# Performance work log

Measured on AMD Instinct MI355X. Metric: run time of the kernel, lower is better.

The kernel has to match this reference:

```python
import jax, jax.numpy as jnp
import numpy as np

B, T, D_MODEL, D_HIDDEN, MAX_SEQLEN = 4, 2048, 1024, 1024, 2048


def setup_inputs() -> dict:
    key = jax.random.key(0)
    ks = jax.random.split(key, 8)
    scale = 0.02  # keep exp() and linear outputs in a sane range
    return {
        "q": jax.random.normal(ks[0], (B, T, D_MODEL), dtype=jnp.float32),
        "k": jax.random.normal(ks[1], (B, T, D_MODEL), dtype=jnp.float32),
        "v": jax.random.normal(ks[2], (B, T, D_MODEL), dtype=jnp.float32),
        "Wq": jax.random.normal(ks[3], (D_HIDDEN, D_MODEL), dtype=jnp.float32) * scale,
        "Wk": jax.random.normal(ks[4], (D_HIDDEN, D_MODEL), dtype=jnp.float32) * scale,
        "Wv": jax.random.normal(ks[5], (D_HIDDEN, D_MODEL), dtype=jnp.float32) * scale,
        "Wo": jax.random.normal(ks[6], (D_MODEL, D_HIDDEN), dtype=jnp.float32) * scale,
        "W_bias": jax.random.normal(ks[7], (MAX_SEQLEN, MAX_SEQLEN), dtype=jnp.float32) * scale,
    }


def reference(q, k, v, Wq, Wk, Wv, Wo, W_bias):
    Ti = q.shape[1]
    Tj = k.shape[1]
    # Linear projections (torch Linear: x @ W.T), bias=False
    Q = jnp.einsum('btm,hm->bth', q, Wq)
    K = jnp.einsum('btm,hm->bth', k, Wk)
    V = jnp.einsum('btm,hm->bth', v, Wv)
    pos_bias = W_bias[:Ti, :Tj][None]              # (1, Ti, Tj)
    # Faithful to original: max over dim 0 (batch dim for K, singleton dim for pos_bias)
    max_key = jnp.max(K, axis=0, keepdims=True)    # (1, Tj, Dh)
    max_pos_bias = jnp.max(pos_bias, axis=0, keepdims=True)  # == pos_bias (dim 0 is size 1)
    exp_key = jnp.exp(K - max_key)                 # (B, Tj, Dh)
    exp_pos_bias = jnp.exp(pos_bias - max_pos_bias)  # all-ones, kept for faithfulness
    num = jnp.einsum('bij,bjd->bid', exp_pos_bias, exp_key * V)
    den = jnp.einsum('bij,bjd->bid', exp_pos_bias, exp_key)
    Yt = jax.nn.sigmoid(Q) * num / den             # (B, Ti, Dh)
    return jnp.einsum('bth,mh->btm', Yt, Wo)
```

## Files before the change

kernel.cpp:

```cpp
#include <hip/hip_runtime.h>
#include <hip/hip_bf16.h>

typedef __bf16 bf16;
typedef __bf16 bf16x8 __attribute__((ext_vector_type(8)));
typedef __bf16 bf16x4 __attribute__((ext_vector_type(4)));
typedef float f32x4 __attribute__((ext_vector_type(4)));
typedef float f32x16 __attribute__((ext_vector_type(16)));

#define B_   4
#define T_   2048
#define DM_  1024
#define DH_  1024
#define MROWS 8192

struct CvtJob { const float* src; bf16* dst; int nf4; };
struct CvtArgs { CvtJob job[7]; };

__global__ __launch_bounds__(256) void cvt_kernel(CvtArgs args) {
  CvtJob jb = args.job[blockIdx.y];
  int base = blockIdx.x * 2048;
  if (base >= jb.nf4) return;
  int t2 = threadIdx.x * 2;
  const float4* s = (const float4*)jb.src;
  float4 a[4][2];
#pragma unroll
  for (int u = 0; u < 4; ++u) {
    a[u][0] = s[base + u * 512 + t2];
    a[u][1] = s[base + u * 512 + t2 + 1];
  }
#pragma unroll
  for (int u = 0; u < 4; ++u) {
    bf16x8 o;
    o[0] = (bf16)a[u][0].x; o[1] = (bf16)a[u][0].y;
    o[2] = (bf16)a[u][0].z; o[3] = (bf16)a[u][0].w;
    o[4] = (bf16)a[u][1].x; o[5] = (bf16)a[u][1].y;
    o[6] = (bf16)a[u][1].z; o[7] = (bf16)a[u][1].w;
    *(bf16x8*)(jb.dst + ((size_t)base + u * 512 + t2) * 4) = o;
  }
}

struct GemmJob { const bf16* A; const bf16* Bw; float* Cf; bf16* Cb; int mode; };
struct GemmArgs { GemmJob job[4]; int N; int K; };

template <int MT>
__global__ __launch_bounds__(256) void gemm_bt(GemmArgs ga) {
  const GemmJob jb = ga.job[blockIdx.z];
  const int N = ga.N, K = ga.K;
  constexpr int TM = MT * 64;
  __shared__ __align__(16) bf16 As[TM * 64];
  __shared__ __align__(16) bf16 Bs[128 * 64];

  const int tid  = threadIdx.x;
  const int lane = tid & 63;
  const int wave = tid >> 6;
  const int wm   = (wave >> 1) * (MT * 32);
  const int wn   = (wave & 1) * 64;

  const int f   = blockIdx.y * 8 + blockIdx.x;
  const int xcd = f & 7;
  const int j   = f >> 3;
  const int bn  = j & 7;
  const int bm  = (j >> 3) * 8 + xcd;
  const int tileM = bm * TM;
  const int tileN = bn * 128;

  f32x16 acc[MT][2] = {};

  const int sr = lane >> 3;

  const char* pa = (const char*)(jb.A  + (size_t)tileM * K);
  const char* pb = (const char*)(jb.Bw + (size_t)tileN * K);
  unsigned int offA[MT * 2], offB[4];
#pragma unroll
  for (int l = 0; l < MT * 2; ++l) {
    int grp = wave * (MT * 2) + l;
    int sc  = (lane & 7) ^ sr ^ (grp & 7);
    offA[l] = (unsigned int)(((grp * 8 + sr) * K + sc * 8) * 2);
  }
#pragma unroll
  for (int l = 0; l < 4; ++l) {
    int grp = wave * 4 + l;
    int sc  = (lane & 7) ^ sr ^ (grp & 7);
    offB[l] = (unsigned int)(((grp * 8 + sr) * K + sc * 8) * 2);
  }

  const int half = lane >> 5;
  const int rc   = lane & 31;

  for (int k0 = 0; k0 < K; k0 += 64) {
#pragma unroll
    for (int l = 0; l < MT * 2; ++l)
      __builtin_amdgcn_global_load_lds(
          (const __attribute__((address_space(1))) void*)(pa + offA[l]),
          (__attribute__((address_space(3))) void*)&As[(wave * (MT * 2) + l) * 512],
          16, 0, 0);
#pragma unroll
    for (int l = 0; l < 4; ++l)
      __builtin_amdgcn_global_load_lds(
          (const __attribute__((address_space(1))) void*)(pb + offB[l]),
          (__attribute__((address_space(3))) void*)&Bs[(wave * 4 + l) * 512],
          16, 0, 0);
    pa += 128;
    pb += 128;
    __syncthreads();

#pragma unroll
    for (int s = 0; s < 2; ++s) {
      bf16x8 af[MT][2], bfr[2][2];
#pragma unroll
      for (int mt = 0; mt < MT; ++mt)
#pragma unroll
        for (int kk = 0; kk < 2; ++kk) {
          int row = wm + mt * 32 + rc;
          int chunk = ((s * 2 + kk) * 2 + half) ^ (row & 7) ^ ((row >> 3) & 7);
          af[mt][kk] = *(const bf16x8*)&As[row * 64 + chunk * 8];
        }
#pragma unroll
      for (int nt = 0; nt < 2; ++nt)
#pragma unroll
        for (int kk = 0; kk < 2; ++kk) {
          int row = wn + nt * 32 + rc;
          int chunk = ((s * 2 + kk) * 2 + half) ^ (row & 7) ^ ((row >> 3) & 7);
          bfr[nt][kk] = *(const bf16x8*)&Bs[row * 64 + chunk * 8];
        }
#pragma unroll
      for (int kk = 0; kk < 2; ++kk)
#pragma unroll
        for (int mt = 0; mt < MT; ++mt)
#pragma unroll
          for (int nt = 0; nt < 2; ++nt)
            acc[mt][nt] = __builtin_amdgcn_mfma_f32_32x32x16_bf16(
                af[mt][kk], bfr[nt][kk], acc[mt][nt], 0, 0, 0);
    }
    __syncthreads();
  }

  const int cn    = rc;
  const int rbase = half * 4;
  if (jb.mode == 0) {
#pragma unroll
    for (int mt = 0; mt < MT; ++mt)
#pragma unroll
      for (int nt = 0; nt < 2; ++nt)
#pragma unroll
        for (int r = 0; r < 16; ++r) {
          int row = tileM + wm + mt * 32 + rbase + (r & 3) + 8 * (r >> 2);
          int col = tileN + wn + nt * 32 + cn;
          jb.Cf[(size_t)row * N + col] = acc[mt][nt][r];
        }
  } else if (jb.mode == 1) {
#pragma unroll
    for (int mt = 0; mt < MT; ++mt)
#pragma unroll
      for (int nt = 0; nt < 2; ++nt)
#pragma unroll
        for (int r = 0; r < 16; ++r) {
          int row = tileM + wm + mt * 32 + rbase + (r & 3) + 8 * (r >> 2);
          int col = tileN + wn + nt * 32 + cn;
          jb.Cb[(size_t)row * N + col] =
              (bf16)(1.f / (1.f + __expf(-acc[mt][nt][r])));
        }
  } else {
#pragma unroll
    for (int mt = 0; mt < MT; ++mt)
#pragma unroll
      for (int nt = 0; nt < 2; ++nt)
#pragma unroll
        for (int r = 0; r < 16; ++r) {
          int row = tileM + wm + mt * 32 + rbase + (r & 3) + 8 * (r >> 2);
          int col = tileN + wn + nt * 32 + cn;
          jb.Cb[(size_t)row * N + col] = (bf16)acc[mt][nt][r];
        }
  }
}

__global__ __launch_bounds__(256) void reduce_kv(
    const bf16* __restrict__ Kb, const bf16* __restrict__ Vb,
    float* __restrict__ part) {
  __shared__ float lds[64 * 128];
  const int t = threadIdx.x;
  const int half = t >> 7;
  const int dt = t & 127;
  const int d = dt * 8;
  const int j0 = blockIdx.x * 8 + half * 4;
  const size_t bs = (size_t)T_ * DH_;
  float n[4][8] = {}, e[4][8] = {};
  for (int jj = j0; jj < j0 + 4; ++jj) {
    size_t off = (size_t)jj * DH_ + d;
    bf16x8 kk[4], vv[4];
#pragma unroll
    for (int b = 0; b < 4; ++b) {
      kk[b] = *(const bf16x8*)(Kb + off + b * bs);
      vv[b] = *(const bf16x8*)(Vb + off + b * bs);
    }
#pragma unroll
    for (int c = 0; c < 8; ++c) {
      float k0 = (float)kk[0][c], k1 = (float)kk[1][c];
      float k2 = (float)kk[2][c], k3 = (float)kk[3][c];
      float m = fmaxf(fmaxf(k0, k1), fmaxf(k2, k3));
      float w0 = __expf(k0 - m), w1 = __expf(k1 - m);
      float w2 = __expf(k2 - m), w3 = __expf(k3 - m);
      e[0][c] += w0; e[1][c] += w1; e[2][c] += w2; e[3][c] += w3;
      n[0][c] += w0 * (float)vv[0][c];
      n[1][c] += w1 * (float)vv[1][c];
      n[2][c] += w2 * (float)vv[2][c];
      n[3][c] += w3 * (float)vv[3][c];
    }
  }
  if (half) {
#pragma unroll
    for (int b = 0; b < 4; ++b)
#pragma unroll
      for (int c = 0; c < 8; ++c) {
        lds[(b * 8 + c) * 128 + dt] = n[b][c];
        lds[(32 + b * 8 + c) * 128 + dt] = e[b][c];
      }
  }
  __syncthreads();
  if (!half) {
    float* po = part + (size_t)blockIdx.x * 8192;
#pragma unroll
    for (int b = 0; b < 4; ++b)
#pragma unroll
      for (int c = 0; c < 8; ++c) {
        po[b * 1024 + d + c] = n[b][c] + lds[(b * 8 + c) * 128 + dt];
        po[4096 + b * 1024 + d + c] = e[b][c] + lds[(32 + b * 8 + c) * 128 + dt];
      }
  }
}

__global__ __launch_bounds__(256) void finish_kv(
    const float* __restrict__ part, float* __restrict__ numden) {
  __shared__ float lds[128];
  const int t = threadIdx.x;
  const int half = t >> 7;
  const int sl = t & 127;
  const int slot = blockIdx.x * 128 + sl;
  float s = 0.f;
  for (int i = half * 128; i < half * 128 + 128; i += 8) {
#pragma unroll
    for (int u = 0; u < 8; ++u)
      s += part[(size_t)(i + u) * 8192 + slot];
  }
  if (half) lds[sl] = s;
  __syncthreads();
  if (!half) numden[slot] = s + lds[sl];
}

__global__ __launch_bounds__(256) void scale_wo(
    const bf16* __restrict__ Wo, const float* __restrict__ numden,
    bf16* __restrict__ out4) {
  const int b = blockIdx.y;
  size_t i = ((size_t)blockIdx.x * 256 + threadIdx.x) * 8;
  int h = (int)(i & (DH_ - 1));
  bf16x8 w = *(const bf16x8*)(Wo + i);
  const float* nu = numden + b * DH_ + h;
  const float* de = numden + 4096 + b * DH_ + h;
  float4 n0 = *(const float4*)nu;
  float4 n1 = *(const float4*)(nu + 4);
  float4 d0 = *(const float4*)de;
  float4 d1 = *(const float4*)(de + 4);
  bf16x8 o;
  o[0] = (bf16)((float)w[0] * n0.x / d0.x);
  o[1] = (bf16)((float)w[1] * n0.y / d0.y);
  o[2] = (bf16)((float)w[2] * n0.z / d0.z);
  o[3] = (bf16)((float)w[3] * n0.w / d0.w);
  o[4] = (bf16)((float)w[4] * n1.x / d1.x);
  o[5] = (bf16)((float)w[5] * n1.y / d1.y);
  o[6] = (bf16)((float)w[6] * n1.z / d1.z);
  o[7] = (bf16)((float)w[7] * n1.w / d1.w);
  *(bf16x8*)(out4 + (size_t)b * ((size_t)DM_ * DH_) + i) = o;
}

extern "C" void kernel_launch(void* const* d_in, const int* in_sizes, int n_in,
                              void* d_out, int out_size, void* d_ws, size_t ws_size,
                              hipStream_t stream) {
  const float* q  = (const float*)d_in[0];
  const float* k  = (const float*)d_in[1];
  const float* v  = (const float*)d_in[2];
  const float* Wq = (const float*)d_in[3];
  const float* Wk = (const float*)d_in[4];
  const float* Wv = (const float*)d_in[5];
  const float* Wo = (const float*)d_in[6];
  float* out = (float*)d_out;

  char* ws = (char*)d_ws;
  size_t off = 0;
  auto alloc = [&](size_t bytes) {
    char* p = ws + off;
    off += (bytes + 255) & ~(size_t)255;
    return p;
  };
  const size_t actN = (size_t)MROWS * DM_;
  const size_t wN   = (size_t)DH_ * DM_;

  bf16* qb  = (bf16*)alloc(actN * 2);
  bf16* kb  = (bf16*)alloc(actN * 2);
  bf16* vb  = (bf16*)alloc(actN * 2);
  bf16* Wqb = (bf16*)alloc(wN * 2);
  bf16* Wkb = (bf16*)alloc(wN * 2);
  bf16* Wvb = (bf16*)alloc(wN * 2);
  bf16* Wob = (bf16*)alloc(wN * 2);
  bf16* Kb  = (bf16*)alloc(actN * 2);
  bf16* Vb  = (bf16*)alloc(actN * 2);
  bf16* Yb  = (bf16*)alloc(actN * 2);
  float* part = (float*)alloc((size_t)256 * 8192 * 4);
  float* numden = (float*)alloc(8192 * 4);
  bf16* Wob4 = (bf16*)part;

  CvtArgs ca;
  ca.job[0] = {q,  qb,  (int)(actN / 4)};
  ca.job[1] = {k,  kb,  (int)(actN / 4)};
  ca.job[2] = {v,  vb,  (int)(actN / 4)};
  ca.job[3] = {Wq, Wqb, (int)(wN / 4)};
  ca.job[4] = {Wk, Wkb, (int)(wN / 4)};
  ca.job[5] = {Wv, Wvb, (int)(wN / 4)};
  ca.job[6] = {Wo, Wob, (int)(wN / 4)};
  cvt_kernel<<<dim3(actN / 4 / 2048, 7), 256, 0, stream>>>(ca);

  GemmArgs g1;
  g1.N = DH_; g1.K = DM_;
  g1.job[0] = {kb, Wkb, nullptr, Kb, 2};
  g1.job[1] = {vb, Wvb, nullptr, Vb, 2};
  g1.job[2] = {qb, Wqb, nullptr, Yb, 1};
  g1.job[3] = {nullptr, nullptr, nullptr, nullptr, 0};
  gemm_bt<2><<<dim3(8, MROWS / 128, 3), 256, 0, stream>>>(g1);

  reduce_kv<<<dim3(256), 256, 0, stream>>>(Kb, Vb, part);
  finish_kv<<<dim3(64), 256, 0, stream>>>(part, numden);

  scale_wo<<<dim3(512, 4), 256, 0, stream>>>(Wob, numden, Wob4);

  GemmArgs g2;
  g2.N = DM_; g2.K = DH_;
  for (int b = 0; b < 4; ++b) {
    g2.job[b] = {Yb + (size_t)b * ((size_t)T_ * DH_),
                 Wob4 + (size_t)b * wN,
                 out + (size_t)b * ((size_t)T_ * DM_),
                 nullptr, 0};
  }
  gemm_bt<1><<<dim3(8, 32, 4), 256, 0, stream>>>(g2);
}
```

Baseline: 269.5 us.

## Fuse K/V projection GEMMs with exp-weighted reduction to skip K/V materialization

```diff
diff --git a/kernel.cpp b/kernel.cpp
--- a/kernel.cpp
+++ b/kernel.cpp
@@ -3,7 +3,6 @@
 
 typedef __bf16 bf16;
 typedef __bf16 bf16x8 __attribute__((ext_vector_type(8)));
-typedef __bf16 bf16x4 __attribute__((ext_vector_type(4)));
 typedef float f32x4 __attribute__((ext_vector_type(4)));
 typedef float f32x16 __attribute__((ext_vector_type(16)));
 
@@ -174,77 +173,151 @@
   }
 }
 
-__global__ __launch_bounds__(256) void reduce_kv(
-    const bf16* __restrict__ Kb, const bf16* __restrict__ Vb,
+__global__ __launch_bounds__(256) void kv_fused(
+    const bf16* __restrict__ Ak, const bf16* __restrict__ Wk,
+    const bf16* __restrict__ Av, const bf16* __restrict__ Wv,
     float* __restrict__ part) {
-  __shared__ float lds[64 * 128];
-  const int t = threadIdx.x;
-  const int half = t >> 7;
-  const int dt = t & 127;
-  const int d = dt * 8;
-  const int j0 = blockIdx.x * 8 + half * 4;
-  const size_t bs = (size_t)T_ * DH_;
-  float n[4][8] = {}, e[4][8] = {};
-  for (int jj = j0; jj < j0 + 4; ++jj) {
-    size_t off = (size_t)jj * DH_ + d;
-    bf16x8 kk[4], vv[4];
-#pragma unroll
-    for (int b = 0; b < 4; ++b) {
-      kk[b] = *(const bf16x8*)(Kb + off + b * bs);
-      vv[b] = *(const bf16x8*)(Vb + off + b * bs);
+  const int K = DM_;
+  __shared__ __align__(16) bf16 As[128 * 64];
+  __shared__ __align__(16) bf16 Bs[128 * 64];
+
+  const int tid  = threadIdx.x;
+  const int lane = tid & 63;
+  const int wave = tid >> 6;
+  const int wm   = (wave >> 1) * 64;
+  const int wn   = (wave & 1) * 64;
+
+  const int f   = blockIdx.y * 8 + blockIdx.x;
+  const int xcd = f & 7;
+  const int j   = f >> 3;
+  const int bn  = j & 7;
+  const int bm  = (j >> 3) * 8 + xcd;
+  const int tileN = bn * 128;
+  const int j0    = bm * 32;
+
+  const int sr   = lane >> 3;
+  const int half = lane >> 5;
+  const int rc   = lane & 31;
+
+  unsigned int offA[4], offB[4];
+#pragma unroll
+  for (int l = 0; l < 4; ++l) {
+    int grp = wave * 4 + l;
+    int tr  = grp * 8 + sr;
+    int sc  = (lane & 7) ^ sr ^ (grp & 7);
+    offA[l] = (unsigned int)((((tr >> 5) * T_ + j0 + (tr & 31)) * K + sc * 8) * 2);
+    offB[l] = (unsigned int)(((grp * 8 + sr) * K + sc * 8) * 2);
+  }
+
+  auto run = [&](const char* pa, const char* pb, f32x16 (&acc)[2][2]) {
+    for (int k0 = 0; k0 < K; k0 += 64) {
+#pragma unroll
+      for (int l = 0; l < 4; ++l)
+        __builtin_amdgcn_global_load_lds(
+            (const __attribute__((address_space(1))) void*)(pa + offA[l]),
+            (__attribute__((address_space(3))) void*)&As[(wave * 4 + l) * 512],
+            16, 0, 0);
+#pragma unroll
+      for (int l = 0; l < 4; ++l)
+        __builtin_amdgcn_global_load_lds(
+            (const __attribute__((address_space(1))) void*)(pb + offB[l]),
+            (__attribute__((address_space(3))) void*)&Bs[(wave * 4 + l) * 512],
+            16, 0, 0);
+      pa += 128;
+      pb += 128;
+      __syncthreads();
+#pragma unroll
+      for (int s = 0; s < 2; ++s) {
+        bf16x8 af[2][2], bfr[2][2];
+#pragma unroll
+        for (int mt = 0; mt < 2; ++mt)
+#pragma unroll
+          for (int kk = 0; kk < 2; ++kk) {
+            int row = wm + mt * 32 + rc;
+            int chunk = ((s * 2 + kk) * 2 + half) ^ (row & 7) ^ ((row >> 3) & 7);
+            af[mt][kk] = *(const bf16x8*)&As[row * 64 + chunk * 8];
+          }
+#pragma unroll
+        for (int nt = 0; nt < 2; ++nt)
+#pragma unroll
+          for (int kk = 0; kk < 2; ++kk) {
+            int row = wn + nt * 32 + rc;
+            int chunk = ((s * 2 + kk) * 2 + half) ^ (row & 7) ^ ((row >> 3) & 7);
+            bfr[nt][kk] = *(const bf16x8*)&Bs[row * 64 + chunk * 8];
+          }
+#pragma unroll
+        for (int kk = 0; kk < 2; ++kk)
+#pragma unroll
+          for (int mt = 0; mt < 2; ++mt)
+#pragma unroll
+            for (int nt = 0; nt < 2; ++nt)
+              acc[mt][nt] = __builtin_amdgcn_mfma_f32_32x32x16_bf16(
+                  af[mt][kk], bfr[nt][kk], acc[mt][nt], 0, 0, 0);
+      }
+      __syncthreads();
     }
-#pragma unroll
-    for (int c = 0; c < 8; ++c) {
-      float k0 = (float)kk[0][c], k1 = (float)kk[1][c];
-      float k2 = (float)kk[2][c], k3 = (float)kk[3][c];
-      float m = fmaxf(fmaxf(k0, k1), fmaxf(k2, k3));
-      float w0 = __expf(k0 - m), w1 = __expf(k1 - m);
-      float w2 = __expf(k2 - m), w3 = __expf(k3 - m);
-      e[0][c] += w0; e[1][c] += w1; e[2][c] += w2; e[3][c] += w3;
-      n[0][c] += w0 * (float)vv[0][c];
-      n[1][c] += w1 * (float)vv[1][c];
-      n[2][c] += w2 * (float)vv[2][c];
-      n[3][c] += w3 * (float)vv[3][c];
+  };
+
+  f32x16 aK[2][2] = {}, aV[2][2] = {};
+  run((const char*)Ak, (const char*)(Wk + (size_t)tileN * K), aK);
+  run((const char*)Av, (const char*)(Wv + (size_t)tileN * K), aV);
+
+  const int rbase = half * 4;
+  float* mx01 = (float*)As;
+  float* mx23 = (float*)Bs;
+#pragma unroll
+  for (int nt = 0; nt < 2; ++nt)
+#pragma unroll
+    for (int r = 0; r < 16; ++r) {
+      float ml = fmaxf(aK[0][nt][r], aK[1][nt][r]);
+      int jloc = rbase + (r & 3) + 8 * (r >> 2);
+      int idx  = (wave & 1) * 2048 + jloc * 64 + nt * 32 + rc;
+      if (wave < 2) mx01[idx] = ml; else mx23[idx] = ml;
     }
-  }
-  if (half) {
-#pragma unroll
-    for (int b = 0; b < 4; ++b)
-#pragma unroll
-      for (int c = 0; c < 8; ++c) {
-        lds[(b * 8 + c) * 128 + dt] = n[b][c];
-        lds[(32 + b * 8 + c) * 128 + dt] = e[b][c];
-      }
-  }
   __syncthreads();
-  if (!half) {
-    float* po = part + (size_t)blockIdx.x * 8192;
-#pragma unroll
-    for (int b = 0; b < 4; ++b)
-#pragma unroll
-      for (int c = 0; c < 8; ++c) {
-        po[b * 1024 + d + c] = n[b][c] + lds[(b * 8 + c) * 128 + dt];
-        po[4096 + b * 1024 + d + c] = e[b][c] + lds[(32 + b * 8 + c) * 128 + dt];
-      }
-  }
+  float sn[2][2] = {{0.f, 0.f}, {0.f, 0.f}};
+  float sd[2][2] = {{0.f, 0.f}, {0.f, 0.f}};
+#pragma unroll
+  for (int nt = 0; nt < 2; ++nt)
+#pragma unroll
+    for (int r = 0; r < 16; ++r) {
+      int jloc = rbase + (r & 3) + 8 * (r >> 2);
+      int idx  = (wave & 1) * 2048 + jloc * 64 + nt * 32 + rc;
+      float mo = (wave < 2) ? mx23[idx] : mx01[idx];
+      float m  = fmaxf(fmaxf(aK[0][nt][r], aK[1][nt][r]), mo);
+      float e0 = __expf(aK[0][nt][r] - m);
+      float e1 = __expf(aK[1][nt][r] - m);
+      sn[0][nt] += e0 * aV[0][nt][r];
+      sn[1][nt] += e1 * aV[1][nt][r];
+      sd[0][nt] += e0;
+      sd[1][nt] += e1;
+    }
+#pragma unroll
+  for (int mt = 0; mt < 2; ++mt)
+#pragma unroll
+    for (int nt = 0; nt < 2; ++nt) {
+      float n = sn[mt][nt] + __shfl_xor(sn[mt][nt], 32, 64);
+      float d = sd[mt][nt] + __shfl_xor(sd[mt][nt], 32, 64);
+      int b    = (wave >> 1) * 2 + mt;
+      int dcol = tileN + wn + nt * 32 + rc;
+      size_t base = (size_t)bm * 8192 + (size_t)b * 1024 + dcol;
+      if (lane < 32) part[base] = n;
+      else           part[base + 4096] = d;
+    }
 }
 
 __global__ __launch_bounds__(256) void finish_kv(
     const float* __restrict__ part, float* __restrict__ numden) {
-  __shared__ float lds[128];
-  const int t = threadIdx.x;
-  const int half = t >> 7;
-  const int sl = t & 127;
-  const int slot = blockIdx.x * 128 + sl;
-  float s = 0.f;
-  for (int i = half * 128; i < half * 128 + 128; i += 8) {
-#pragma unroll
-    for (int u = 0; u < 8; ++u)
-      s += part[(size_t)(i + u) * 8192 + slot];
-  }
-  if (half) lds[sl] = s;
-  __syncthreads();
-  if (!half) numden[slot] = s + lds[sl];
+  int slot = blockIdx.x * 256 + threadIdx.x;
+  float s0 = 0.f, s1 = 0.f, s2 = 0.f, s3 = 0.f;
+#pragma unroll
+  for (int i = 0; i < 64; i += 4) {
+    s0 += part[(size_t)(i + 0) * 8192 + slot];
+    s1 += part[(size_t)(i + 1) * 8192 + slot];
+    s2 += part[(size_t)(i + 2) * 8192 + slot];
+    s3 += part[(size_t)(i + 3) * 8192 + slot];
+  }
+  numden[slot] = (s0 + s1) + (s2 + s3);
 }
 
 __global__ __launch_bounds__(256) void scale_wo(
@@ -301,12 +374,10 @@
   bf16* Wkb = (bf16*)alloc(wN * 2);
   bf16* Wvb = (bf16*)alloc(wN * 2);
   bf16* Wob = (bf16*)alloc(wN * 2);
-  bf16* Kb  = (bf16*)alloc(actN * 2);
-  bf16* Vb  = (bf16*)alloc(actN * 2);
   bf16* Yb  = (bf16*)alloc(actN * 2);
-  float* part = (float*)alloc((size_t)256 * 8192 * 4);
+  float* part = (float*)alloc((size_t)64 * 8192 * 4);
   float* numden = (float*)alloc(8192 * 4);
-  bf16* Wob4 = (bf16*)part;
+  bf16* Wob4 = (bf16*)alloc((size_t)B_ * wN * 2);
 
   CvtArgs ca;
   ca.job[0] = {q,  qb,  (int)(actN / 4)};
@@ -320,14 +391,15 @@
 
   GemmArgs g1;
   g1.N = DH_; g1.K = DM_;
-  g1.job[0] = {kb, Wkb, nullptr, Kb, 2};
-  g1.job[1] = {vb, Wvb, nullptr, Vb, 2};
-  g1.job[2] = {qb, Wqb, nullptr, Yb, 1};
+  g1.job[0] = {qb, Wqb, nullptr, Yb, 1};
+  g1.job[1] = {nullptr, nullptr, nullptr, nullptr, 0};
+  g1.job[2] = {nullptr, nullptr, nullptr, nullptr, 0};
   g1.job[3] = {nullptr, nullptr, nullptr, nullptr, 0};
-  gemm_bt<2><<<dim3(8, MROWS / 128, 3), 256, 0, stream>>>(g1);
-
-  reduce_kv<<<dim3(256), 256, 0, stream>>>(Kb, Vb, part);
-  finish_kv<<<dim3(64), 256, 0, stream>>>(part, numden);
+  gemm_bt<2><<<dim3(8, 64, 1), 256, 0, stream>>>(g1);
+
+  kv_fused<<<dim3(8, 64), 256, 0, stream>>>(kb, Wkb, vb, Wvb, part);
+
+  finish_kv<<<dim3(32), 256, 0, stream>>>(part, numden);
 
   scale_wo<<<dim3(512, 4), 256, 0, stream>>>(Wob, numden, Wob4);
 
```

Measured after the change: 286.7 us. +6.4%, slower.
